# Kernel tuning notes

Measured on AMD Instinct MI355X. Metric: run time of the kernel, lower is better.

The kernel has to match this reference:

```python
import jax, jax.numpy as jnp
import numpy as np

MARGIN = 0.5


def _pairwise_sqdist(a, b):
    # ||a_i - b_j||^2 = |a_i|^2 + |b_j|^2 - 2 a_i . b_j  -> [N, N]
    a2 = jnp.sum(a * a, axis=1)
    b2 = jnp.sum(b * b, axis=1)
    return a2[:, None] + b2[None, :] - 2.0 * (a @ b.T)


def setup_inputs() -> dict:
    key = jax.random.key(0)
    k1, k2 = jax.random.split(key)
    N, D = 4096, 256
    pair1 = jax.random.normal(k1, (N, D), dtype=jnp.float32)
    pair2 = jax.random.normal(k2, (N, D), dtype=jnp.float32)
    return {"pair1": pair1, "pair2": pair2}


def reference(pair1, pair2):
    N = pair1.shape[0]
    d11 = _pairwise_sqdist(pair1, pair1)          # dist(p1_i, p1_j)
    d12 = _pairwise_sqdist(pair1, pair2)          # dist(p1_i, p2_j)
    dist_ap = jnp.diagonal(d12)                   # ||p1_i - p2_i||^2, [N]
    off_diag = 1.0 - jnp.eye(N, dtype=pair1.dtype)  # exclude j == i
    hinge = (jax.nn.relu(dist_ap[:, None] - d11 + MARGIN)
             + jax.nn.relu(dist_ap[:, None] - d12 + MARGIN))
    losses = jnp.sum(hinge * off_diag)
    cnt = N * (N - 1)
    return losses / cnt
```

## Files before the change

kernel.cpp:

```cpp
#include <hip/hip_runtime.h>

#define NN 4096
#define DD 256
#define MARGIN 0.5f

typedef __attribute__((ext_vector_type(8))) short bf16x8;
typedef __attribute__((ext_vector_type(4))) float f32x4;

__device__ inline unsigned short f32_to_bf16_rne(float v) {
    unsigned int b = __float_as_uint(v);
    b += 0x7FFFu + ((b >> 16) & 1u);
    return (unsigned short)(b >> 16);
}

__global__ __launch_bounds__(256) void stats_convert(
    const float* __restrict__ p1, const float* __restrict__ p2,
    unsigned short* __restrict__ pb, float* __restrict__ nb,
    float* __restrict__ ai)
{
    const int wave = threadIdx.x >> 6;
    const int lane = threadIdx.x & 63;
    const int row  = blockIdx.x * 4 + wave;

    const float4 x = *(const float4*)&p1[(size_t)row * DD + lane * 4];
    const float4 y = *(const float4*)&p2[(size_t)row * DD + lane * 4];

    ushort4 xb, yb;
    xb.x = f32_to_bf16_rne(x.x); xb.y = f32_to_bf16_rne(x.y);
    xb.z = f32_to_bf16_rne(x.z); xb.w = f32_to_bf16_rne(x.w);
    yb.x = f32_to_bf16_rne(y.x); yb.y = f32_to_bf16_rne(y.y);
    yb.z = f32_to_bf16_rne(y.z); yb.w = f32_to_bf16_rne(y.w);
    *(ushort4*)&pb[(size_t)row * DD + lane * 4] = xb;
    *(ushort4*)&pb[(size_t)(NN + row) * DD + lane * 4] = yb;

    float s1 = x.x*x.x + x.y*x.y + x.z*x.z + x.w*x.w;
    float s2 = y.x*y.x + y.y*y.y + y.z*y.z + y.w*y.w;
    float dx = x.x-y.x, dy = x.y-y.y, dz = x.z-y.z, dw = x.w-y.w;
    float sa = dx*dx + dy*dy + dz*dz + dw*dw;

    #pragma unroll
    for (int off = 32; off > 0; off >>= 1) {
        s1 += __shfl_down(s1, off);
        s2 += __shfl_down(s2, off);
        sa += __shfl_down(sa, off);
    }
    if (lane == 0) {
        nb[row]      = s1;
        nb[NN + row] = s2;
        ai[row]      = sa - s1 + MARGIN;
    }
}

__global__ __launch_bounds__(256) void gemm_hinge(
    const unsigned short* __restrict__ pb,
    const float* __restrict__ nb, const float* __restrict__ ai,
    float* __restrict__ partial)
{
    __shared__ unsigned short As[2][128 * 64];
    __shared__ unsigned short Bs[2][128 * 64];
    __shared__ float wsum[4];

    const int t    = threadIdx.x;
    const int lane = t & 63;
    const int wave = t >> 6;
    const int wm   = wave >> 1;
    const int wn   = wave & 1;
    const int i0   = blockIdx.y * 128;
    const int j0   = blockIdx.x * 128;

    const int lr = lane & 15;
    const int lk = (lane >> 4) * 8;

    const int srow = ((wave * 4) << 3) >> 3;
    (void)srow;

    f32x4 acc[4][4];
    #pragma unroll
    for (int m = 0; m < 4; ++m)
        #pragma unroll
        for (int n = 0; n < 4; ++n)
            acc[m][n] = (f32x4){0.f, 0.f, 0.f, 0.f};

    auto stage = [&](int sel, int kc) {
        #pragma unroll
        for (int q = 0; q < 4; ++q) {
            const int g   = wave * 4 + q;
            const int c   = g * 64 + lane;
            const int row = c >> 3;
            const int k8  = c & 7;
            const unsigned short* ga = pb + (size_t)(i0 + row) * DD + kc + k8 * 8;
            const unsigned short* gb = pb + (size_t)(j0 + row) * DD + kc + k8 * 8;
            __builtin_amdgcn_global_load_lds(
                (const __attribute__((address_space(1))) unsigned int*)ga,
                (__attribute__((address_space(3))) unsigned int*)&As[sel][g * 512],
                16, 0, 0);
            __builtin_amdgcn_global_load_lds(
                (const __attribute__((address_space(1))) unsigned int*)gb,
                (__attribute__((address_space(3))) unsigned int*)&Bs[sel][g * 512],
                16, 0, 0);
        }
    };

    stage(0, 0);
    __syncthreads();

    int sel = 0;
    for (int ks = 0; ks < 4; ++ks) {
        if (ks < 3) stage(sel ^ 1, (ks + 1) * 64);

        #pragma unroll
        for (int kq = 0; kq < 2; ++kq) {
            bf16x8 a[4], b[4];
            #pragma unroll
            for (int m = 0; m < 4; ++m)
                a[m] = *(const bf16x8*)&As[sel][(wm * 64 + m * 16 + lr) * 64 + kq * 32 + lk];
            #pragma unroll
            for (int n = 0; n < 4; ++n)
                b[n] = *(const bf16x8*)&Bs[sel][(wn * 64 + n * 16 + lr) * 64 + kq * 32 + lk];
            #pragma unroll
            for (int m = 0; m < 4; ++m)
                #pragma unroll
                for (int n = 0; n < 4; ++n)
                    acc[m][n] = __builtin_amdgcn_mfma_f32_16x16x32_bf16(
                        a[m], b[n], acc[m][n], 0, 0, 0);
        }
        __syncthreads();
        sel ^= 1;
    }

    const int cj = lane & 15;
    const int r0 = (lane >> 4) * 4;
    float lsum = 0.f;
    #pragma unroll
    for (int m = 0; m < 4; ++m) {
        const int ibase = i0 + wm * 64 + m * 16 + r0;
        float aiv[4];
        #pragma unroll
        for (int r = 0; r < 4; ++r) aiv[r] = ai[ibase + r];
        #pragma unroll
        for (int n = 0; n < 4; ++n) {
            const int j = j0 + wn * 64 + n * 16 + cj;
            const float nbj = nb[j];
            #pragma unroll
            for (int r = 0; r < 4; ++r) {
                const int i = ibase + r;
                float h = fmaf(2.f, acc[m][n][r], aiv[r] - nbj);
                h = fmaxf(h, 0.f);
                if (j != i && j != i + NN) lsum += h;
            }
        }
    }

    #pragma unroll
    for (int off = 32; off > 0; off >>= 1) lsum += __shfl_down(lsum, off);
    if (lane == 0) wsum[wave] = lsum;
    __syncthreads();
    if (t == 0)
        partial[blockIdx.y * gridDim.x + blockIdx.x] =
            wsum[0] + wsum[1] + wsum[2] + wsum[3];
}

__global__ __launch_bounds__(256) void final_reduce(
    const float* __restrict__ partial, float* __restrict__ out,
    int n, float scale)
{
    const int t = threadIdx.x;
    float s = 0.f;
    for (int i = t; i < n; i += 256) s += partial[i];
    #pragma unroll
    for (int off = 32; off > 0; off >>= 1) s += __shfl_down(s, off);
    __shared__ float w[4];
    if ((t & 63) == 0) w[t >> 6] = s;
    __syncthreads();
    if (t == 0) out[0] = (w[0] + w[1] + w[2] + w[3]) * scale;
}

extern "C" void kernel_launch(void* const* d_in, const int* in_sizes, int n_in,
                              void* d_out, int out_size, void* d_ws, size_t ws_size,
                              hipStream_t stream) {
    const float* p1 = (const float*)d_in[0];
    const float* p2 = (const float*)d_in[1];
    float* out = (float*)d_out;

    char* ws = (char*)d_ws;
    unsigned short* pb = (unsigned short*)ws;
    float* nb      = (float*)(ws + (size_t)2 * NN * DD * 2);
    float* ai      = nb + 2 * NN;
    float* partial = ai + NN;

    stats_convert<<<NN / 4, 256, 0, stream>>>(p1, p2, pb, nb, ai);
    gemm_hinge<<<dim3(64, 32), 256, 0, stream>>>(pb, nb, ai, partial);
    const float scale = 1.0f / ((float)NN * (float)(NN - 1));
    final_reduce<<<1, 256, 0, stream>>>(partial, out, 64 * 32, scale);
}
```

Baseline: 42.65 us.

## Keep A stripe in registers and stream full-K B tiles across eight column tiles

The GEMM-hinge kernel becomes a persistent-style grid of 256 blocks of 512 threads. Each block holds its 128-row A stripe (full K=256) in registers and loops over 8 column tiles of 128. Each B tile is staged with full K into double-buffered LDS using an XOR swizzle to avoid bank conflicts, and block-to-stripe mapping is arranged for L2 locality. This removes repeated A staging and the per-tile K-loop synchronisation, at the cost of heavy register use (128 VGPRs for A fragments) and 128KB of LDS per block, which limits occupancy.

```diff
diff --git a/kernel.cpp b/kernel.cpp
--- a/kernel.cpp
+++ b/kernel.cpp
@@ -51,113 +51,129 @@
     }
 }
 
-__global__ __launch_bounds__(256) void gemm_hinge(
+__global__ __launch_bounds__(512, 2) void gemm_hinge(
     const unsigned short* __restrict__ pb,
     const float* __restrict__ nb, const float* __restrict__ ai,
     float* __restrict__ partial)
 {
-    __shared__ unsigned short As[2][128 * 64];
-    __shared__ unsigned short Bs[2][128 * 64];
-    __shared__ float wsum[4];
+    __shared__ unsigned short Bs[2][128 * 256];
+    __shared__ float wsum[8];
 
     const int t    = threadIdx.x;
     const int lane = t & 63;
     const int wave = t >> 6;
-    const int wm   = wave >> 1;
-    const int wn   = wave & 1;
-    const int i0   = blockIdx.y * 128;
-    const int j0   = blockIdx.x * 128;
+    const int wm   = wave >> 2;
+    const int wn   = wave & 3;
+
+    const int bid     = blockIdx.x;
+    const int istripe = (bid & 7) * 4 + (bid >> 6);
+    const int jgroup  = (bid >> 3) & 7;
+    const int i0      = istripe * 128;
 
     const int lr = lane & 15;
-    const int lk = (lane >> 4) * 8;
-
-    const int srow = ((wave * 4) << 3) >> 3;
-    (void)srow;
-
-    f32x4 acc[4][4];
+    const int l4 = lane >> 4;
+    const int lk = l4 * 8;
+
+    bf16x8 a[4][8];
+    #pragma unroll
+    for (int m = 0; m < 4; ++m) {
+        const unsigned short* ar = pb + (size_t)(i0 + wm * 64 + m * 16 + lr) * DD;
+        #pragma unroll
+        for (int kq = 0; kq < 8; ++kq)
+            a[m][kq] = *(const bf16x8*)(ar + kq * 32 + lk);
+    }
+
+    const int r0 = l4 * 4;
+    float aiv[4][4];
     #pragma unroll
     for (int m = 0; m < 4; ++m)
         #pragma unroll
-        for (int n = 0; n < 4; ++n)
-            acc[m][n] = (f32x4){0.f, 0.f, 0.f, 0.f};
-
-    auto stage = [&](int sel, int kc) {
-        #pragma unroll
-        for (int q = 0; q < 4; ++q) {
-            const int g   = wave * 4 + q;
-            const int c   = g * 64 + lane;
-            const int row = c >> 3;
-            const int k8  = c & 7;
-            const unsigned short* ga = pb + (size_t)(i0 + row) * DD + kc + k8 * 8;
-            const unsigned short* gb = pb + (size_t)(j0 + row) * DD + kc + k8 * 8;
+        for (int r = 0; r < 4; ++r)
+            aiv[m][r] = ai[i0 + wm * 64 + m * 16 + r0 + r];
+
+    auto stage = [&](int sel, int jt) {
+        const int j0 = jt * 128;
+        #pragma unroll
+        for (int q = 0; q < 8; ++q) {
+            const int cbase = q * 512 + wave * 64;
+            const int c     = cbase + lane;
+            const int row   = c >> 5;
+            const int cw    = c & 31;
+            const unsigned short* g =
+                pb + (size_t)(j0 + row) * DD + ((cw ^ (row & 7)) * 8);
             __builtin_amdgcn_global_load_lds(
-                (const __attribute__((address_space(1))) unsigned int*)ga,
-                (__attribute__((address_space(3))) unsigned int*)&As[sel][g * 512],
-                16, 0, 0);
-            __builtin_amdgcn_global_load_lds(
-                (const __attribute__((address_space(1))) unsigned int*)gb,
-                (__attribute__((address_space(3))) unsigned int*)&Bs[sel][g * 512],
+                (const __attribute__((address_space(1))) unsigned int*)g,
+                (__attribute__((address_space(3))) unsigned int*)&Bs[sel][cbase * 8],
                 16, 0, 0);
         }
     };
 
-    stage(0, 0);
+    const int jt0 = jgroup * 8;
+    float lsum = 0.f;
+
+    stage(0, jt0);
     __syncthreads();
 
     int sel = 0;
-    for (int ks = 0; ks < 4; ++ks) {
-        if (ks < 3) stage(sel ^ 1, (ks + 1) * 64);
-
-        #pragma unroll
-        for (int kq = 0; kq < 2; ++kq) {
-            bf16x8 a[4], b[4];
-            #pragma unroll
-            for (int m = 0; m < 4; ++m)
-                a[m] = *(const bf16x8*)&As[sel][(wm * 64 + m * 16 + lr) * 64 + kq * 32 + lk];
-            #pragma unroll
-            for (int n = 0; n < 4; ++n)
-                b[n] = *(const bf16x8*)&Bs[sel][(wn * 64 + n * 16 + lr) * 64 + kq * 32 + lk];
+    for (int jj = 0; jj < 8; ++jj) {
+        const int jt = jt0 + jj;
+        const int j0 = jt * 128;
+        if (jj < 7) stage(sel ^ 1, jt + 1);
+
+        f32x4 acc[4][2];
+        #pragma unroll
+        for (int m = 0; m < 4; ++m)
+            #pragma unroll
+            for (int n = 0; n < 2; ++n)
+                acc[m][n] = (f32x4){0.f, 0.f, 0.f, 0.f};
+
+        #pragma unroll
+        for (int kq = 0; kq < 8; ++kq) {
+            bf16x8 b[2];
+            #pragma unroll
+            for (int n = 0; n < 2; ++n) {
+                const int row = wn * 32 + n * 16 + lr;
+                const int cl  = kq * 4 + l4;
+                b[n] = *(const bf16x8*)&Bs[sel][row * 256 + ((cl ^ (row & 7)) * 8)];
+            }
             #pragma unroll
             for (int m = 0; m < 4; ++m)
                 #pragma unroll
-                for (int n = 0; n < 4; ++n)
+                for (int n = 0; n < 2; ++n)
                     acc[m][n] = __builtin_amdgcn_mfma_f32_16x16x32_bf16(
-                        a[m], b[n], acc[m][n], 0, 0, 0);
+                        a[m][kq], b[n], acc[m][n], 0, 0, 0);
         }
+
+        #pragma unroll
+        for (int n = 0; n < 2; ++n) {
+            const int j   = j0 + wn * 32 + n * 16 + lr;
+            const float nbj = nb[j];
+            #pragma unroll
+            for (int m = 0; m < 4; ++m) {
+                #pragma unroll
+                for (int r = 0; r < 4; ++r) {
+                    const int i = i0 + wm * 64 + m * 16 + r0 + r;
+                    float h = fmaf(2.f, acc[m][n][r], aiv[m][r] - nbj);
+                    h = fmaxf(h, 0.f);
+                    if (j != i && j != i + NN) lsum += h;
+                }
+            }
+        }
+
         __syncthreads();
         sel ^= 1;
-    }
-
-    const int cj = lane & 15;
-    const int r0 = (lane >> 4) * 4;
-    float lsum = 0.f;
-    #pragma unroll
-    for (int m = 0; m < 4; ++m) {
-        const int ibase = i0 + wm * 64 + m * 16 + r0;
-        float aiv[4];
-        #pragma unroll
-        for (int r = 0; r < 4; ++r) aiv[r] = ai[ibase + r];
-        #pragma unroll
-        for (int n = 0; n < 4; ++n) {
-            const int j = j0 + wn * 64 + n * 16 + cj;
-            const float nbj = nb[j];
-            #pragma unroll
-            for (int r = 0; r < 4; ++r) {
-                const int i = ibase + r;
-                float h = fmaf(2.f, acc[m][n][r], aiv[r] - nbj);
-                h = fmaxf(h, 0.f);
-                if (j != i && j != i + NN) lsum += h;
-            }
-        }
     }
 
     #pragma unroll
     for (int off = 32; off > 0; off >>= 1) lsum += __shfl_down(lsum, off);
     if (lane == 0) wsum[wave] = lsum;
     __syncthreads();
-    if (t == 0)
-        partial[blockIdx.y * gridDim.x + blockIdx.x] =
-            wsum[0] + wsum[1] + wsum[2] + wsum[3];
+    if (t == 0) {
+        float s = 0.f;
+        #pragma unroll
+        for (int w = 0; w < 8; ++w) s += wsum[w];
+        partial[bid] = s;
+    }
 }
 
 __global__ __launch_bounds__(256) void final_reduce(
@@ -189,7 +205,7 @@
     float* partial = ai + NN;
 
     stats_convert<<<NN / 4, 256, 0, stream>>>(p1, p2, pb, nb, ai);
-    gemm_hinge<<<dim3(64, 32), 256, 0, stream>>>(pb, nb, ai, partial);
+    gemm_hinge<<<256, 512, 0, stream>>>(pb, nb, ai, partial);
     const float scale = 1.0f / ((float)NN * (float)(NN - 1));
-    final_reduce<<<1, 256, 0, stream>>>(partial, out, 64 * 32, scale);
-}
+    final_reduce<<<1, 256, 0, stream>>>(partial, out, 256, scale);
+}
```

Result: faster. 39.40 us (-7.6%).
